# Performance work log

Measured on AMD Instinct MI355X. Metric: run time of the kernel, lower is better.

Reference implementation:

```python
import jax, jax.numpy as jnp
import numpy as np

N = 1_000_000
D = 128
P = 16384  # number of person segments


def setup_inputs() -> dict:
    key = jax.random.key(0)
    k1, k2, k3, k4, k5 = jax.random.split(key, 5)
    x = jax.random.normal(k1, (N, D), dtype=jnp.float32)
    person_ids = jnp.sort(jax.random.randint(k2, (N,), 0, P, dtype=jnp.int32))
    dh = D // 4
    # attention MLP params: Linear(D, D//4) -> tanh -> Linear(D//4, 1)
    W1 = jax.random.normal(k3, (D, dh), dtype=jnp.float32) / np.sqrt(D)
    b1 = jnp.zeros((dh,), dtype=jnp.float32)
    W2 = jax.random.normal(k4, (dh, 1), dtype=jnp.float32) / np.sqrt(dh)
    b2 = jnp.zeros((1,), dtype=jnp.float32)
    return {"x": x, "person_ids": person_ids, "W1": W1, "b1": b1, "W2": W2, "b2": b2}


def reference(x, person_ids, W1, b1, W2, b2):
    # attention scores per node: (N,)
    scores = (jnp.tanh(x @ W1 + b1) @ W2 + b2).squeeze(-1)
    # per-segment numerically-stable softmax (one fused O(N) pass)
    seg_max = jax.ops.segment_max(scores, person_ids, num_segments=P)
    seg_max = jnp.where(jnp.isfinite(seg_max), seg_max, 0.0)  # guard empty segments
    e = jnp.exp(scores - seg_max[person_ids])
    denom = jax.ops.segment_sum(e, person_ids, num_segments=P)
    denom = jnp.where(denom == 0.0, 1.0, denom)
    w = e / denom[person_ids]                     # (N,)
    pooled = jax.ops.segment_sum(w[:, None] * x, person_ids, num_segments=P)  # (P, D)
    pooled_pids = jnp.arange(P, dtype=person_ids.dtype)
    return pooled, pooled_pids
```

## Files before the change

kernel.cpp:

```cpp
#include <hip/hip_runtime.h>

#define D_  128
#define DH_ 32

typedef __attribute__((ext_vector_type(8))) short bf16x8;
typedef __attribute__((ext_vector_type(4))) float f32x4;

__device__ __forceinline__ short f2bf(float f) {
    unsigned u = __float_as_uint(f);
    unsigned r = (u + 0x7FFF + ((u >> 16) & 1)) >> 16;
    return (short)r;
}

__global__ __launch_bounds__(256, 4) void tap_main(
    const float* __restrict__ x,
    const int*   __restrict__ pid,
    const float* __restrict__ W1,
    const float* __restrict__ b1,
    const float* __restrict__ W2,
    const float* __restrict__ b2,
    float* __restrict__ out,
    int N, int P)
{
    __shared__ int   sid[256];
    __shared__ float se[256];

    const int tid  = threadIdx.x;
    const int lane = tid & 63;
    const int wave = tid >> 6;
    const int row0 = blockIdx.x * 256;
    const int rb   = wave * 64;

    { int gr = row0 + tid; if (gr > N - 1) gr = N - 1; sid[tid] = pid[gr]; }

    const int n16  = lane & 15;
    const int quad = lane >> 4;

    bf16x8 bfrag[4][2];
    #pragma unroll
    for (int kt = 0; kt < 4; ++kt)
        #pragma unroll
        for (int jt = 0; jt < 2; ++jt) {
            const float* wp = W1 + (kt * 32 + quad * 8) * DH_ + jt * 16 + n16;
            #pragma unroll
            for (int i = 0; i < 8; ++i) bfrag[kt][jt][i] = f2bf(wp[i * DH_]);
        }

    f32x4 acc[4][2] = {};

    for (int kt = 0; kt < 4; ++kt) {
        bf16x8 afrag[4];
        #pragma unroll
        for (int mt = 0; mt < 4; ++mt) {
            int r = row0 + rb + mt * 16 + n16; if (r > N - 1) r = N - 1;
            const float* ap = x + (size_t)r * D_ + kt * 32 + quad * 8;
            float4 v0 = *(const float4*)ap;
            float4 v1 = *(const float4*)(ap + 4);
            afrag[mt][0] = f2bf(v0.x); afrag[mt][1] = f2bf(v0.y);
            afrag[mt][2] = f2bf(v0.z); afrag[mt][3] = f2bf(v0.w);
            afrag[mt][4] = f2bf(v1.x); afrag[mt][5] = f2bf(v1.y);
            afrag[mt][6] = f2bf(v1.z); afrag[mt][7] = f2bf(v1.w);
        }
        #pragma unroll
        for (int mt = 0; mt < 4; ++mt)
            #pragma unroll
            for (int jt = 0; jt < 2; ++jt)
                acc[mt][jt] = __builtin_amdgcn_mfma_f32_16x16x32_bf16(
                    afrag[mt], bfrag[kt][jt], acc[mt][jt], 0, 0, 0);
    }

    const float b2v = b2[0];
    float w2v[2], b1v[2];
    #pragma unroll
    for (int jt = 0; jt < 2; ++jt) {
        w2v[jt] = W2[jt * 16 + n16];
        b1v[jt] = b1[jt * 16 + n16];
    }

    #pragma unroll
    for (int mt = 0; mt < 4; ++mt) {
        #pragma unroll
        for (int q = 0; q < 4; ++q) {
            float s = 0.f;
            #pragma unroll
            for (int jt = 0; jt < 2; ++jt) {
                float h = acc[mt][jt][q] + b1v[jt];
                h = fminf(fmaxf(h, -15.f), 15.f);
                float z = __expf(2.f * h);
                float t = 1.f - 2.f / (z + 1.f);
                s = fmaf(t, w2v[jt], s);
            }
            s += __shfl_xor(s, 1);
            s += __shfl_xor(s, 2);
            s += __shfl_xor(s, 4);
            s += __shfl_xor(s, 8);
            if (n16 == 0) {
                int rloc = rb + mt * 16 + quad * 4 + q;
                int gr   = row0 + rloc;
                se[rloc] = (gr < N) ? __expf(s + b2v) : 0.f;
            }
        }
    }

    float a0 = 0.f, a1 = 0.f, ad = 0.f;
    int   cur = sid[rb];
    #pragma unroll
    for (int r = rb; r < rb + 64; ++r) {
        int sg = sid[r];
        if (sg != cur) {
            atomicAdd(&out[cur * D_ + 2 * lane],     a0);
            atomicAdd(&out[cur * D_ + 2 * lane + 1], a1);
            if (lane == 0) atomicAdd(&out[P * D_ + cur], ad);
            a0 = a1 = ad = 0.f;
            cur = sg;
        }
        float ev = se[r];
        int gr = row0 + r; if (gr > N - 1) gr = N - 1;
        const float2 xv = *(const float2*)&x[(size_t)gr * D_ + 2 * lane];
        a0 = fmaf(ev, xv.x, a0);
        a1 = fmaf(ev, xv.y, a1);
        ad += ev;
    }
    atomicAdd(&out[cur * D_ + 2 * lane],     a0);
    atomicAdd(&out[cur * D_ + 2 * lane + 1], a1);
    if (lane == 0) atomicAdd(&out[P * D_ + cur], ad);
}

__global__ __launch_bounds__(128) void tap_finalize(float* __restrict__ out, int P)
{
    const int p = blockIdx.x;
    const int f = threadIdx.x;
    float den = out[P * D_ + p];
    den = (den == 0.f) ? 1.f : den;
    float v = out[p * D_ + f];
    __syncthreads();
    out[p * D_ + f] = v / den;
    if (f == 0) out[P * D_ + p] = (float)p;
}

extern "C" void kernel_launch(void* const* d_in, const int* in_sizes, int n_in,
                              void* d_out, int out_size, void* d_ws, size_t ws_size,
                              hipStream_t stream)
{
    const float* x   = (const float*)d_in[0];
    const int*   pid = (const int*)d_in[1];
    const float* W1  = (const float*)d_in[2];
    const float* b1  = (const float*)d_in[3];
    const float* W2  = (const float*)d_in[4];
    const float* b2  = (const float*)d_in[5];
    float* out = (float*)d_out;

    const int N = in_sizes[0] / D_;
    const int P = out_size / (D_ + 1);

    hipMemsetAsync(d_out, 0, (size_t)out_size * sizeof(float), stream);

    const int blocks = (N + 255) / 256;
    tap_main<<<blocks, 256, 0, stream>>>(x, pid, W1, b1, W2, b2, out, N, P);
    tap_finalize<<<P, 128, 0, stream>>>(out, P);
}
```

Before: 752.0 us.

## Assign one wave per segment using precomputed offsets, drop atomics and finalize

A new kernel computes segment start offsets from the sorted ids, and the main kernel now assigns one wave per person segment. Each wave scores and accumulates its segment's rows, then normalizes and writes the result directly. This removes the memset, the atomic adds and the separate finalize kernel. In exchange, load balance depends on segment sizes, partial 16-row tiles waste MFMA work, and bf16 packing now truncates instead of rounding.

```diff
diff --git a/kernel.cpp b/kernel.cpp
--- a/kernel.cpp
+++ b/kernel.cpp
@@ -6,15 +6,25 @@
 typedef __attribute__((ext_vector_type(8))) short bf16x8;
 typedef __attribute__((ext_vector_type(4))) float f32x4;
 
-__device__ __forceinline__ short f2bf(float f) {
-    unsigned u = __float_as_uint(f);
-    unsigned r = (u + 0x7FFF + ((u >> 16) & 1)) >> 16;
-    return (short)r;
+__device__ __forceinline__ unsigned pk_bf16(float lo, float hi) {
+    return __builtin_amdgcn_perm(__float_as_uint(hi), __float_as_uint(lo), 0x07060302u);
 }
 
-__global__ __launch_bounds__(256, 4) void tap_main(
+__global__ __launch_bounds__(256) void seg_offsets(
+    const int* __restrict__ pid, int* __restrict__ start, int N, int P)
+{
+    int i = blockIdx.x * 256 + threadIdx.x;
+    if (i >= N) return;
+    int p1 = pid[i];
+    int p0 = (i == 0) ? -1 : pid[i - 1];
+    for (int p = p0 + 1; p <= p1; ++p) start[p] = i;
+    if (i == N - 1)
+        for (int p = p1 + 1; p <= P; ++p) start[p] = N;
+}
+
+__global__ __launch_bounds__(256, 4) void tap_seg(
     const float* __restrict__ x,
-    const int*   __restrict__ pid,
+    const int*   __restrict__ start,
     const float* __restrict__ W1,
     const float* __restrict__ b1,
     const float* __restrict__ W2,
@@ -22,19 +32,16 @@
     float* __restrict__ out,
     int N, int P)
 {
-    __shared__ int   sid[256];
-    __shared__ float se[256];
+    __shared__ float seW[4][64];
 
     const int tid  = threadIdx.x;
     const int lane = tid & 63;
     const int wave = tid >> 6;
-    const int row0 = blockIdx.x * 256;
-    const int rb   = wave * 64;
-
-    { int gr = row0 + tid; if (gr > N - 1) gr = N - 1; sid[tid] = pid[gr]; }
-
+    const int p    = blockIdx.x * 4 + wave;
     const int n16  = lane & 15;
     const int quad = lane >> 4;
+
+    if (p >= P) return;
 
     bf16x8 bfrag[4][2];
     #pragma unroll
@@ -42,100 +49,98 @@
         #pragma unroll
         for (int jt = 0; jt < 2; ++jt) {
             const float* wp = W1 + (kt * 32 + quad * 8) * DH_ + jt * 16 + n16;
+            union { bf16x8 v; unsigned u[4]; } bf;
             #pragma unroll
-            for (int i = 0; i < 8; ++i) bfrag[kt][jt][i] = f2bf(wp[i * DH_]);
+            for (int i = 0; i < 4; ++i)
+                bf.u[i] = pk_bf16(wp[(2 * i) * DH_], wp[(2 * i + 1) * DH_]);
+            bfrag[kt][jt] = bf.v;
+        }
+    float w2v[2] = { W2[n16], W2[16 + n16] };
+    float b1v[2] = { b1[n16], b1[16 + n16] };
+    const float b2v = b2[0];
+
+    int s0 = __builtin_amdgcn_readfirstlane(start[p]);
+    int s1 = __builtin_amdgcn_readfirstlane(start[p + 1]);
+
+    const int fo = 2 * lane;
+    float a0 = 0.f, a1 = 0.f, ad = 0.f;
+
+    for (int r0 = s0; r0 < s1; r0 += 64) {
+        const int nrows  = min(64, s1 - r0);
+        const int mtiles = (nrows + 15) >> 4;
+
+        f32x4 acc[4][2] = {};
+        #pragma unroll
+        for (int kt = 0; kt < 4; ++kt) {
+            bf16x8 afrag[4];
+            for (int mt = 0; mt < mtiles; ++mt) {
+                int r = r0 + mt * 16 + n16; if (r > N - 1) r = N - 1;
+                const float* ap = x + (size_t)r * D_ + kt * 32 + quad * 8;
+                float4 v0 = *(const float4*)ap;
+                float4 v1 = *(const float4*)(ap + 4);
+                union { bf16x8 v; unsigned u[4]; } af;
+                af.u[0] = pk_bf16(v0.x, v0.y);
+                af.u[1] = pk_bf16(v0.z, v0.w);
+                af.u[2] = pk_bf16(v1.x, v1.y);
+                af.u[3] = pk_bf16(v1.z, v1.w);
+                afrag[mt] = af.v;
+            }
+            for (int mt = 0; mt < mtiles; ++mt) {
+                acc[mt][0] = __builtin_amdgcn_mfma_f32_16x16x32_bf16(
+                    afrag[mt], bfrag[kt][0], acc[mt][0], 0, 0, 0);
+                acc[mt][1] = __builtin_amdgcn_mfma_f32_16x16x32_bf16(
+                    afrag[mt], bfrag[kt][1], acc[mt][1], 0, 0, 0);
+            }
         }
 
-    f32x4 acc[4][2] = {};
+        for (int mt = 0; mt < mtiles; ++mt) {
+            #pragma unroll
+            for (int q = 0; q < 4; ++q) {
+                float s = 0.f;
+                #pragma unroll
+                for (int jt = 0; jt < 2; ++jt) {
+                    float h = acc[mt][jt][q] + b1v[jt];
+                    h = fminf(fmaxf(h, -15.f), 15.f);
+                    float z = __expf(2.f * h);
+                    float t = 1.f - 2.f / (z + 1.f);
+                    s = fmaf(t, w2v[jt], s);
+                }
+                s += __shfl_xor(s, 1);
+                s += __shfl_xor(s, 2);
+                s += __shfl_xor(s, 4);
+                s += __shfl_xor(s, 8);
+                if (n16 == 0)
+                    seW[wave][mt * 16 + quad * 4 + q] = __expf(s + b2v);
+            }
+        }
 
-    for (int kt = 0; kt < 4; ++kt) {
-        bf16x8 afrag[4];
-        #pragma unroll
-        for (int mt = 0; mt < 4; ++mt) {
-            int r = row0 + rb + mt * 16 + n16; if (r > N - 1) r = N - 1;
-            const float* ap = x + (size_t)r * D_ + kt * 32 + quad * 8;
-            float4 v0 = *(const float4*)ap;
-            float4 v1 = *(const float4*)(ap + 4);
-            afrag[mt][0] = f2bf(v0.x); afrag[mt][1] = f2bf(v0.y);
-            afrag[mt][2] = f2bf(v0.z); afrag[mt][3] = f2bf(v0.w);
-            afrag[mt][4] = f2bf(v1.x); afrag[mt][5] = f2bf(v1.y);
-            afrag[mt][6] = f2bf(v1.z); afrag[mt][7] = f2bf(v1.w);
+        const int rend = r0 + nrows;
+        int r = r0;
+        for (; r + 4 <= rend; r += 4) {
+            float e0 = seW[wave][r - r0 + 0];
+            float e1 = seW[wave][r - r0 + 1];
+            float e2 = seW[wave][r - r0 + 2];
+            float e3 = seW[wave][r - r0 + 3];
+            float2 x0 = *(const float2*)&x[(size_t)(r + 0) * D_ + fo];
+            float2 x1 = *(const float2*)&x[(size_t)(r + 1) * D_ + fo];
+            float2 x2 = *(const float2*)&x[(size_t)(r + 2) * D_ + fo];
+            float2 x3 = *(const float2*)&x[(size_t)(r + 3) * D_ + fo];
+            a0 = fmaf(e0, x0.x, a0); a1 = fmaf(e0, x0.y, a1); ad += e0;
+            a0 = fmaf(e1, x1.x, a0); a1 = fmaf(e1, x1.y, a1); ad += e1;
+            a0 = fmaf(e2, x2.x, a0); a1 = fmaf(e2, x2.y, a1); ad += e2;
+            a0 = fmaf(e3, x3.x, a0); a1 = fmaf(e3, x3.y, a1); ad += e3;
         }
-        #pragma unroll
-        for (int mt = 0; mt < 4; ++mt)
-            #pragma unroll
-            for (int jt = 0; jt < 2; ++jt)
-                acc[mt][jt] = __builtin_amdgcn_mfma_f32_16x16x32_bf16(
-                    afrag[mt], bfrag[kt][jt], acc[mt][jt], 0, 0, 0);
-    }
-
-    const float b2v = b2[0];
-    float w2v[2], b1v[2];
-    #pragma unroll
-    for (int jt = 0; jt < 2; ++jt) {
-        w2v[jt] = W2[jt * 16 + n16];
-        b1v[jt] = b1[jt * 16 + n16];
-    }
-
-    #pragma unroll
-    for (int mt = 0; mt < 4; ++mt) {
-        #pragma unroll
-        for (int q = 0; q < 4; ++q) {
-            float s = 0.f;
-            #pragma unroll
-            for (int jt = 0; jt < 2; ++jt) {
-                float h = acc[mt][jt][q] + b1v[jt];
-                h = fminf(fmaxf(h, -15.f), 15.f);
-                float z = __expf(2.f * h);
-                float t = 1.f - 2.f / (z + 1.f);
-                s = fmaf(t, w2v[jt], s);
-            }
-            s += __shfl_xor(s, 1);
-            s += __shfl_xor(s, 2);
-            s += __shfl_xor(s, 4);
-            s += __shfl_xor(s, 8);
-            if (n16 == 0) {
-                int rloc = rb + mt * 16 + quad * 4 + q;
-                int gr   = row0 + rloc;
-                se[rloc] = (gr < N) ? __expf(s + b2v) : 0.f;
-            }
+        for (; r < rend; ++r) {
+            float ev = seW[wave][r - r0];
+            float2 xv = *(const float2*)&x[(size_t)r * D_ + fo];
+            a0 = fmaf(ev, xv.x, a0); a1 = fmaf(ev, xv.y, a1); ad += ev;
         }
     }
 
-    float a0 = 0.f, a1 = 0.f, ad = 0.f;
-    int   cur = sid[rb];
-    #pragma unroll
-    for (int r = rb; r < rb + 64; ++r) {
-        int sg = sid[r];
-        if (sg != cur) {
-            atomicAdd(&out[cur * D_ + 2 * lane],     a0);
-            atomicAdd(&out[cur * D_ + 2 * lane + 1], a1);
-            if (lane == 0) atomicAdd(&out[P * D_ + cur], ad);
-            a0 = a1 = ad = 0.f;
-            cur = sg;
-        }
-        float ev = se[r];
-        int gr = row0 + r; if (gr > N - 1) gr = N - 1;
-        const float2 xv = *(const float2*)&x[(size_t)gr * D_ + 2 * lane];
-        a0 = fmaf(ev, xv.x, a0);
-        a1 = fmaf(ev, xv.y, a1);
-        ad += ev;
-    }
-    atomicAdd(&out[cur * D_ + 2 * lane],     a0);
-    atomicAdd(&out[cur * D_ + 2 * lane + 1], a1);
-    if (lane == 0) atomicAdd(&out[P * D_ + cur], ad);
-}
-
-__global__ __launch_bounds__(128) void tap_finalize(float* __restrict__ out, int P)
-{
-    const int p = blockIdx.x;
-    const int f = threadIdx.x;
-    float den = out[P * D_ + p];
-    den = (den == 0.f) ? 1.f : den;
-    float v = out[p * D_ + f];
-    __syncthreads();
-    out[p * D_ + f] = v / den;
-    if (f == 0) out[P * D_ + p] = (float)p;
+    float den = (ad == 0.f) ? 1.f : ad;
+    out[(size_t)p * D_ + fo]     = a0 / den;
+    out[(size_t)p * D_ + fo + 1] = a1 / den;
+    if (lane == 0) out[(size_t)P * D_ + p] = (float)p;
 }
 
 extern "C" void kernel_launch(void* const* d_in, const int* in_sizes, int n_in,
@@ -153,9 +158,8 @@
     const int N = in_sizes[0] / D_;
     const int P = out_size / (D_ + 1);
 
-    hipMemsetAsync(d_out, 0, (size_t)out_size * sizeof(float), stream);
+    int* start = (int*)d_ws;
 
-    const int blocks = (N + 255) / 256;
-    tap_main<<<blocks, 256, 0, stream>>>(x, pid, W1, b1, W2, b2, out, N, P);
-    tap_finalize<<<P, 128, 0, stream>>>(out, P);
+    seg_offsets<<<(N + 255) / 256, 256, 0, stream>>>(pid, start, N, P);
+    tap_seg<<<(P + 3) / 4, 256, 0, stream>>>(x, start, W1, b1, W2, b2, out, N, P);
 }
```

Result: slower. 1.604 ms (+113.3%).
